# Kernel optimization log

Hardware: AMD Instinct MI355X
Metric: run time of the kernel (lower is better)

The kernel has to match this reference:

```python
import jax, jax.numpy as jnp
import numpy as np

SEQ_LEN = 1
INPUT = 2048
HIDDEN = 2048
CLASSES = 10
K = int(np.floor(np.sqrt(HIDDEN)))            # avgKernelSize = 45
NUM_EH = (HIDDEN - K) // K + 1                # 45 pooled features
LENGTHS = (32, 128, 512)                      # EHlengths (window sizes)
EST_DIM = NUM_EH * len(LENGTHS) * 2           # mean + variance per (feature, window)
B = 8192


def setup_inputs() -> dict:
    key = jax.random.key(0)
    ks = jax.random.split(key, 7)
    s = 1.0 / np.sqrt(HIDDEN)
    u = lambda k, shape: jax.random.uniform(k, shape, jnp.float32, -s, s)
    return {
        "x": jax.random.normal(ks[0], (B, SEQ_LEN, INPUT), jnp.float32),
        "W_ih": u(ks[1], (HIDDEN, INPUT)),
        "W_hh": u(ks[2], (HIDDEN, HIDDEN)),
        "b_ih": u(ks[3], (HIDDEN,)),
        "b_hh": u(ks[4], (HIDDEN,)),
        "W_lin": u(ks[5], (CLASSES, HIDDEN + EST_DIM)),
        "b_lin": u(ks[6], (CLASSES,)),
    }


def _sliding_stats(pooled):
    """Causal sliding-window mean/variance over the batch/stream axis.

    pooled: (B, F). Returns (B, F, J, 2) with [..., 0]=mean, [..., 1]=var.
    This is the exact quantity the VarEH exponential histograms approximate
    (streaming mean/variance over the last L elements added).
    """
    n = pooled.shape[0]
    cs = jnp.cumsum(pooled, axis=0)
    cs2 = jnp.cumsum(pooled * pooled, axis=0)
    idx = jnp.arange(n)
    outs = []
    for L in LENGTHS:  # small fixed set of window lengths
        zpad = jnp.zeros((L,) + pooled.shape[1:], pooled.dtype)
        cs_l = jnp.concatenate([zpad, cs], axis=0)[:n]
        cs2_l = jnp.concatenate([zpad, cs2], axis=0)[:n]
        cnt = jnp.minimum(idx + 1, L).astype(pooled.dtype)[:, None]
        m = (cs - cs_l) / cnt
        v = (cs2 - cs2_l) / cnt - m * m
        outs.append(jnp.stack([m, v], axis=-1))  # (B, F, 2)
    return jnp.stack(outs, axis=2)  # (B, F, J, 2)


def reference(x, W_ih, W_hh, b_ih, b_hh, W_lin, b_lin):
    b = x.shape[0]
    # Elman RNN, batch_first, h0 = 0. Precompute input projection for all steps.
    xw = jnp.einsum("bsi,hi->bsh", x, W_ih) + b_ih + b_hh  # (B, S, H)

    def step(h, xt):
        h = jnp.tanh(xt + h @ W_hh.T)
        return h, h

    h0 = jnp.zeros((b, HIDDEN), x.dtype)
    _, hs = jax.lax.scan(step, h0, jnp.swapaxes(xw, 0, 1))  # (S, B, H)
    rnn_out = hs[-1]  # (B, H); with seq_len=1 this equals squeeze(rnn_out)

    # AvgPool1d(kernel=K, stride=K) over hidden dim -> (B, NUM_EH)
    pooled = rnn_out[:, : NUM_EH * K].reshape(b, NUM_EH, K).mean(axis=-1)

    # Streaming mean/var estimates across the batch stream (VarEH semantics)
    est = _sliding_stats(pooled).reshape(b, EST_DIM)

    lin_in = jnp.concatenate([rnn_out, est], axis=1)  # (B, H + EST_DIM)
    logits = lin_in @ W_lin.T + b_lin
    return jax.nn.softmax(logits, axis=1)
```

## Files before the change

### kernel.cpp

```cpp
#include <hip/hip_runtime.h>
#include <hip/hip_bf16.h>
#include <math.h>

typedef short s16x8 __attribute__((ext_vector_type(8)));
typedef float f32x4 __attribute__((ext_vector_type(4)));

__device__ inline unsigned short f2bf(float x) {
    unsigned int u = __float_as_uint(x);
    unsigned int r = (u + 0x7fffu + ((u >> 16) & 1u)) >> 16;
    return (unsigned short)r;
}
__device__ inline float bf2f(unsigned short u) {
    return __uint_as_float(((unsigned int)u) << 16);
}

__device__ inline float fast_tanh(float x) {
    float e = __expf(2.0f * x);
    return 1.0f - 2.0f * __builtin_amdgcn_rcpf(e + 1.0f);
}

__global__ void cvtprep_kernel(const float* __restrict__ x,
                               const float* __restrict__ W_ih,
                               const float* __restrict__ W_lin,
                               unsigned short* __restrict__ xb,
                               unsigned short* __restrict__ wb,
                               unsigned short* __restrict__ wlb) {
    int blk = blockIdx.x;
    int tid = threadIdx.x;
    if (blk < 16384) {
        int i = blk * 256 + tid;
        float4 v = ((const float4*)x)[i];
        ushort4 o; o.x = f2bf(v.x); o.y = f2bf(v.y); o.z = f2bf(v.z); o.w = f2bf(v.w);
        ((ushort4*)xb)[i] = o;
    } else if (blk < 20480) {
        int i = (blk - 16384) * 256 + tid;
        float4 v = ((const float4*)W_ih)[i];
        ushort4 o; o.x = f2bf(v.x); o.y = f2bf(v.y); o.z = f2bf(v.z); o.w = f2bf(v.w);
        ((ushort4*)wb)[i] = o;
    } else {
        int idx = (blk - 20480) * 256 + tid;
        if (idx < 37376) {
            int c = idx / 2336, k = idx - c * 2336;
            float v = (c < 10 && k < 2318) ? W_lin[c * 2318 + k] : 0.f;
            wlb[idx] = f2bf(v);
        }
    }
}

__global__ __launch_bounds__(256) void gemm_tanh_kernel(
    const unsigned short* __restrict__ A, const unsigned short* __restrict__ Bm,
    const float* __restrict__ b_ih, const float* __restrict__ b_hh,
    unsigned short* __restrict__ Hb)
{
    __shared__ unsigned short As[128 * 32];
    __shared__ unsigned short Bs[128 * 32];

    const int tid  = threadIdx.x;
    const int lane = tid & 63;
    const int wave = tid >> 6;
    const int row0 = blockIdx.x * 128;
    const int col0 = blockIdx.y * 128;
    const int wr = (wave >> 1) * 64;
    const int wc = (wave & 1) * 64;
    const int quad = lane >> 4;
    const int mrow = lane & 15;

    f32x4 acc[4][4];
#pragma unroll
    for (int i = 0; i < 4; ++i)
#pragma unroll
        for (int j = 0; j < 4; ++j)
            acc[i][j] = f32x4{0.f, 0.f, 0.f, 0.f};

    for (int k0 = 0; k0 < 2048; k0 += 32) {
        __syncthreads();
#pragma unroll
        for (int i = 0; i < 2; ++i) {
            int t = i * 256 + tid;
            int r = t >> 2, c = t & 3;
            int cg = c ^ ((r >> 1) & 3);
            const unsigned short* gp = A + (size_t)(row0 + r) * 2048 + k0 + cg * 8;
            __builtin_amdgcn_global_load_lds(
                (const __attribute__((address_space(1))) void*)gp,
                (__attribute__((address_space(3))) void*)(&As[t * 8]), 16, 0, 0);
        }
#pragma unroll
        for (int i = 0; i < 2; ++i) {
            int t = i * 256 + tid;
            int r = t >> 2, c = t & 3;
            int cg = c ^ ((r >> 1) & 3);
            const unsigned short* gp = Bm + (size_t)(col0 + r) * 2048 + k0 + cg * 8;
            __builtin_amdgcn_global_load_lds(
                (const __attribute__((address_space(1))) void*)gp,
                (__attribute__((address_space(3))) void*)(&Bs[t * 8]), 16, 0, 0);
        }
        __syncthreads();

        s16x8 af[4], bfr[4];
#pragma unroll
        for (int i = 0; i < 4; ++i) {
            int R = wr + i * 16 + mrow;
            int slot = quad ^ ((R >> 1) & 3);
            af[i] = *(const s16x8*)(&As[R * 32 + slot * 8]);
        }
#pragma unroll
        for (int j = 0; j < 4; ++j) {
            int R = wc + j * 16 + mrow;
            int slot = quad ^ ((R >> 1) & 3);
            bfr[j] = *(const s16x8*)(&Bs[R * 32 + slot * 8]);
        }
#pragma unroll
        for (int i = 0; i < 4; ++i)
#pragma unroll
            for (int j = 0; j < 4; ++j)
                acc[i][j] = __builtin_amdgcn_mfma_f32_16x16x32_bf16(
                    af[i], bfr[j], acc[i][j], 0, 0, 0);
    }

    float bias[4];
#pragma unroll
    for (int j = 0; j < 4; ++j) {
        int gc = col0 + wc + j * 16 + mrow;
        bias[j] = b_ih[gc] + b_hh[gc];
    }
#pragma unroll
    for (int i = 0; i < 4; ++i) {
#pragma unroll
        for (int r = 0; r < 4; ++r) {
            int grow = row0 + wr + i * 16 + quad * 4 + r;
#pragma unroll
            for (int j = 0; j < 4; ++j) {
                int gc = col0 + wc + j * 16 + mrow;
                float v = acc[i][j][r] + bias[j];
                Hb[(size_t)grow * 2048 + gc] = f2bf(fast_tanh(v));
            }
        }
    }
}

__global__ __launch_bounds__(256) void pool_kernel(
    const unsigned short* __restrict__ Hb, float* __restrict__ pooled_t) {
    __shared__ unsigned short hs[8 * 2048];
    __shared__ float outs[45 * 8];
    int b0 = blockIdx.x * 8;
    int tid = threadIdx.x;
    const ushort4* src = (const ushort4*)(Hb + (size_t)b0 * 2048);
    ushort4* dst = (ushort4*)hs;
    for (int i = tid; i < 4096; i += 256) dst[i] = src[i];
    __syncthreads();
    for (int o = tid; o < 360; o += 256) {
        int f = o % 45, r = o / 45;
        const unsigned short* row = hs + r * 2048 + f * 45;
        float s = 0.f;
#pragma unroll
        for (int k = 0; k < 45; ++k) s += bf2f(row[k]);
        outs[f * 8 + r] = s * (1.0f / 45.0f);
    }
    __syncthreads();
    for (int o = tid; o < 360; o += 256) {
        int f = o >> 3, r = o & 7;
        pooled_t[f * 8192 + b0 + r] = outs[o];
    }
}

__global__ __launch_bounds__(256) void scan_kernel(
    const float* __restrict__ pooled_t,
    float* __restrict__ cs_t, float* __restrict__ cs2_t) {
    __shared__ float t1[256], t2[256];
    int f = blockIdx.x;
    int tid = threadIdx.x;
    const float* p = pooled_t + f * 8192;
    int base = tid * 32;
    float loc[32];
    float s1 = 0.f, s2 = 0.f;
#pragma unroll
    for (int i = 0; i < 32; ++i) {
        float v = p[base + i];
        loc[i] = v; s1 += v; s2 += v * v;
    }
    t1[tid] = s1; t2[tid] = s2;
    __syncthreads();
    for (int d = 1; d < 256; d <<= 1) {
        float a1 = (tid >= d) ? t1[tid - d] : 0.f;
        float a2 = (tid >= d) ? t2[tid - d] : 0.f;
        __syncthreads();
        t1[tid] += a1; t2[tid] += a2;
        __syncthreads();
    }
    float r1 = t1[tid] - s1, r2 = t2[tid] - s2;
    float* c1 = cs_t + f * 8192;
    float* c2 = cs2_t + f * 8192;
#pragma unroll
    for (int i = 0; i < 32; ++i) {
        float v = loc[i];
        r1 += v; r2 += v * v;
        c1[base + i] = r1; c2[base + i] = r2;
    }
}

#define ESTRIDE 290
__global__ __launch_bounds__(256) void final_kernel(
    const unsigned short* __restrict__ Hb,
    const float* __restrict__ cs_t, const float* __restrict__ cs2_t,
    const unsigned short* __restrict__ Wb, const float* __restrict__ b_lin,
    float* __restrict__ out) {
    __shared__ unsigned short Es[32 * ESTRIDE];
    __shared__ float comb[2 * 16 * 17];
    int tid = threadIdx.x;
    int lane = tid & 63;
    int wave = tid >> 6;
    int b0 = blockIdx.x * 32;

    for (int i = tid; i < 135 * 32; i += 256) {
        int fj = i >> 5, r = i & 31;
        int f = fj / 3, j = fj - 3 * f;
        int b = b0 + r;
        int L = (j == 0) ? 32 : (j == 1) ? 128 : 512;
        const float* c1 = cs_t + f * 8192;
        const float* c2 = cs2_t + f * 8192;
        float a1 = c1[b], a2 = c2[b];
        float p1 = 0.f, p2 = 0.f;
        if (b >= L) { p1 = c1[b - L]; p2 = c2[b - L]; }
        float cnt = (float)((b + 1 < L) ? (b + 1) : L);
        float m = (a1 - p1) / cnt;
        float v = (a2 - p2) / cnt - m * m;
        int d0 = f * 6 + j * 2;
        Es[r * ESTRIDE + d0]     = f2bf(m);
        Es[r * ESTRIDE + d0 + 1] = f2bf(v);
    }
    for (int i = tid; i < 32 * 18; i += 256) {
        int r = i / 18, d = 270 + i % 18;
        Es[r * ESTRIDE + d] = 0;
    }
    __syncthreads();

    const int t = wave >> 1;
    const int kh = wave & 1;
    const int quad = lane >> 4;
    const int mrow = lane & 15;
    const int rowt = b0 + t * 16;

    f32x4 acc = f32x4{0.f, 0.f, 0.f, 0.f};
    const unsigned short* arow = Hb + (size_t)(rowt + mrow) * 2048 + kh * 1024 + quad * 8;
    const unsigned short* brow = Wb + (size_t)mrow * 2336 + kh * 1024 + quad * 8;
#pragma unroll 4
    for (int k = 0; k < 1024; k += 32) {
        s16x8 a = *(const s16x8*)(arow + k);
        s16x8 b = *(const s16x8*)(brow + k);
        acc = __builtin_amdgcn_mfma_f32_16x16x32_bf16(a, b, acc, 0, 0, 0);
    }
    if (kh) {
        const unsigned short* erow = Es + (t * 16 + mrow) * ESTRIDE + quad * 8;
        const unsigned short* wrow = Wb + (size_t)mrow * 2336 + 2048 + quad * 8;
#pragma unroll
        for (int k = 0; k < 288; k += 32) {
            s16x8 a = *(const s16x8*)(erow + k);
            s16x8 b = *(const s16x8*)(wrow + k);
            acc = __builtin_amdgcn_mfma_f32_16x16x32_bf16(a, b, acc, 0, 0, 0);
        }
    }

    float* cb = comb + t * 272;
    if (kh == 0) {
#pragma unroll
        for (int r = 0; r < 4; ++r) cb[(quad * 4 + r) * 17 + mrow] = acc[r];
    }
    __syncthreads();
    if (kh == 1) {
#pragma unroll
        for (int r = 0; r < 4; ++r) cb[(quad * 4 + r) * 17 + mrow] += acc[r];
    }
    __syncthreads();

    if (tid < 32) {
        const float* base = comb + (tid >> 4) * 272 + (tid & 15) * 17;
        float lg[10];
        float mx = -1e30f;
#pragma unroll
        for (int c = 0; c < 10; ++c) {
            lg[c] = base[c] + b_lin[c];
            mx = fmaxf(mx, lg[c]);
        }
        float s = 0.f;
#pragma unroll
        for (int c = 0; c < 10; ++c) { lg[c] = expf(lg[c] - mx); s += lg[c]; }
        float inv = 1.0f / s;
#pragma unroll
        for (int c = 0; c < 10; ++c) out[(size_t)(b0 + tid) * 10 + c] = lg[c] * inv;
    }
}

extern "C" void kernel_launch(void* const* d_in, const int* in_sizes, int n_in,
                              void* d_out, int out_size, void* d_ws, size_t ws_size,
                              hipStream_t stream) {
    const float* x     = (const float*)d_in[0];
    const float* W_ih  = (const float*)d_in[1];
    const float* b_ih  = (const float*)d_in[3];
    const float* b_hh  = (const float*)d_in[4];
    const float* W_lin = (const float*)d_in[5];
    const float* b_lin = (const float*)d_in[6];
    float* out = (float*)d_out;

    char* ws = (char*)d_ws;
    unsigned short* xb  = (unsigned short*)(ws);
    unsigned short* wb  = (unsigned short*)(ws + 33554432);
    unsigned short* Hb  = (unsigned short*)(ws + 41943040);
    float* pooled_t     = (float*)(ws + 75497472);
    float* cs_t         = (float*)(ws + 76972032);
    float* cs2_t        = (float*)(ws + 78446592);
    unsigned short* wlb = (unsigned short*)(ws + 79921152);

    cvtprep_kernel<<<20626, 256, 0, stream>>>(x, W_ih, W_lin, xb, wb, wlb);
    dim3 ggrid(64, 16);
    gemm_tanh_kernel<<<ggrid, 256, 0, stream>>>(xb, wb, b_ih, b_hh, Hb);
    pool_kernel<<<1024, 256, 0, stream>>>(Hb, pooled_t);
    scan_kernel<<<45, 256, 0, stream>>>(pooled_t, cs_t, cs2_t);
    final_kernel<<<256, 256, 0, stream>>>(Hb, cs_t, cs2_t, wlb, b_lin, out);
}
```

Before: 253.2 us.

## Rewrite RNN input GEMM as 256x256 double-buffered pipelined MFMA kernel

```diff
diff --git a/kernel.cpp b/kernel.cpp
--- a/kernel.cpp
+++ b/kernel.cpp
@@ -47,91 +47,171 @@
     }
 }
 
-__global__ __launch_bounds__(256) void gemm_tanh_kernel(
+
+#define MFMA_(a, b, c) __builtin_amdgcn_mfma_f32_16x16x32_bf16(a, b, c, 0, 0, 0)
+
+__device__ inline s16x8 frag_ld(const unsigned short* hbase, int row, int ksub, int quad) {
+    int slot = (ksub * 4 + quad) ^ (row & 7);
+    return *(const s16x8*)(hbase + row * 64 + slot * 8);
+}
+
+__device__ inline void stage_u(const unsigned short* __restrict__ gmat, int half,
+                               int rowoff, int kt, unsigned short* lmat, int tid) {
+    int r = tid >> 3, s = tid & 7;
+    int lr = rowoff + r;
+    int ks = (s ^ (lr & 7)) << 3;
+    const unsigned short* gp = gmat + (size_t)(half * 128 + lr) * 2048 + kt * 64 + ks;
+    __builtin_amdgcn_global_load_lds(
+        (const __attribute__((address_space(1))) void*)gp,
+        (__attribute__((address_space(3))) void*)(lmat + half * 8192 + lr * 64 + s * 8),
+        16, 0, 0);
+}
+
+#define LOAD_AQ(q)                                                       \
+    af0 = frag_ld(Ah, (q) * 32 +      mrow, 0, quad);                    \
+    af1 = frag_ld(Ah, (q) * 32 + 16 + mrow, 0, quad);                    \
+    af2 = frag_ld(Ah, (q) * 32 +      mrow, 1, quad);                    \
+    af3 = frag_ld(Ah, (q) * 32 + 16 + mrow, 1, quad);
+
+#define MFMA_Q(q)                                                        \
+    acc[(q)*2 + 0][0] = MFMA_(af0, bf00, acc[(q)*2 + 0][0]);             \
+    acc[(q)*2 + 0][1] = MFMA_(af0, bf01, acc[(q)*2 + 0][1]);             \
+    acc[(q)*2 + 0][2] = MFMA_(af0, bf02, acc[(q)*2 + 0][2]);             \
+    acc[(q)*2 + 0][3] = MFMA_(af0, bf03, acc[(q)*2 + 0][3]);             \
+    acc[(q)*2 + 1][0] = MFMA_(af1, bf00, acc[(q)*2 + 1][0]);             \
+    acc[(q)*2 + 1][1] = MFMA_(af1, bf01, acc[(q)*2 + 1][1]);             \
+    acc[(q)*2 + 1][2] = MFMA_(af1, bf02, acc[(q)*2 + 1][2]);             \
+    acc[(q)*2 + 1][3] = MFMA_(af1, bf03, acc[(q)*2 + 1][3]);             \
+    acc[(q)*2 + 0][0] = MFMA_(af2, bf10, acc[(q)*2 + 0][0]);             \
+    acc[(q)*2 + 0][1] = MFMA_(af2, bf11, acc[(q)*2 + 0][1]);             \
+    acc[(q)*2 + 0][2] = MFMA_(af2, bf12, acc[(q)*2 + 0][2]);             \
+    acc[(q)*2 + 0][3] = MFMA_(af2, bf13, acc[(q)*2 + 0][3]);             \
+    acc[(q)*2 + 1][0] = MFMA_(af3, bf10, acc[(q)*2 + 1][0]);             \
+    acc[(q)*2 + 1][1] = MFMA_(af3, bf11, acc[(q)*2 + 1][1]);             \
+    acc[(q)*2 + 1][2] = MFMA_(af3, bf12, acc[(q)*2 + 1][2]);             \
+    acc[(q)*2 + 1][3] = MFMA_(af3, bf13, acc[(q)*2 + 1][3]);
+
+#define PHASE_CORE(q)                                                    \
+    __builtin_amdgcn_s_barrier();                                        \
+    asm volatile("s_waitcnt lgkmcnt(0)" ::: "memory");                   \
+    __builtin_amdgcn_s_setprio(1);                                       \
+    MFMA_Q(q);                                                           \
+    __builtin_amdgcn_s_setprio(0);
+
+__global__ __launch_bounds__(512) void gemm_tanh_kernel(
     const unsigned short* __restrict__ A, const unsigned short* __restrict__ Bm,
     const float* __restrict__ b_ih, const float* __restrict__ b_hh,
     unsigned short* __restrict__ Hb)
 {
-    __shared__ unsigned short As[128 * 32];
-    __shared__ unsigned short Bs[128 * 32];
+    __shared__ __align__(16) unsigned short lds[2][2][16384];
 
     const int tid  = threadIdx.x;
     const int lane = tid & 63;
     const int wave = tid >> 6;
-    const int row0 = blockIdx.x * 128;
-    const int col0 = blockIdx.y * 128;
-    const int wr = (wave >> 1) * 64;
-    const int wc = (wave & 1) * 64;
+    const int wgid = blockIdx.x;
+    const int cblk = wgid & 7;
+    const int rblk = wgid >> 3;
+    const int row0 = rblk * 256;
+    const int col0 = cblk * 256;
+    const int wm   = wave >> 2;
+    const int wn   = wave & 3;
     const int quad = lane >> 4;
     const int mrow = lane & 15;
-
-    f32x4 acc[4][4];
-#pragma unroll
-    for (int i = 0; i < 4; ++i)
-#pragma unroll
-        for (int j = 0; j < 4; ++j)
-            acc[i][j] = f32x4{0.f, 0.f, 0.f, 0.f};
-
-    for (int k0 = 0; k0 < 2048; k0 += 32) {
-        __syncthreads();
-#pragma unroll
-        for (int i = 0; i < 2; ++i) {
-            int t = i * 256 + tid;
-            int r = t >> 2, c = t & 3;
-            int cg = c ^ ((r >> 1) & 3);
-            const unsigned short* gp = A + (size_t)(row0 + r) * 2048 + k0 + cg * 8;
-            __builtin_amdgcn_global_load_lds(
-                (const __attribute__((address_space(1))) void*)gp,
-                (__attribute__((address_space(3))) void*)(&As[t * 8]), 16, 0, 0);
-        }
-#pragma unroll
-        for (int i = 0; i < 2; ++i) {
-            int t = i * 256 + tid;
-            int r = t >> 2, c = t & 3;
-            int cg = c ^ ((r >> 1) & 3);
-            const unsigned short* gp = Bm + (size_t)(col0 + r) * 2048 + k0 + cg * 8;
-            __builtin_amdgcn_global_load_lds(
-                (const __attribute__((address_space(1))) void*)gp,
-                (__attribute__((address_space(3))) void*)(&Bs[t * 8]), 16, 0, 0);
-        }
-        __syncthreads();
-
-        s16x8 af[4], bfr[4];
-#pragma unroll
-        for (int i = 0; i < 4; ++i) {
-            int R = wr + i * 16 + mrow;
-            int slot = quad ^ ((R >> 1) & 3);
-            af[i] = *(const s16x8*)(&As[R * 32 + slot * 8]);
-        }
-#pragma unroll
-        for (int j = 0; j < 4; ++j) {
-            int R = wc + j * 16 + mrow;
-            int slot = quad ^ ((R >> 1) & 3);
-            bfr[j] = *(const s16x8*)(&Bs[R * 32 + slot * 8]);
-        }
-#pragma unroll
-        for (int i = 0; i < 4; ++i)
-#pragma unroll
-            for (int j = 0; j < 4; ++j)
-                acc[i][j] = __builtin_amdgcn_mfma_f32_16x16x32_bf16(
-                    af[i], bfr[j], acc[i][j], 0, 0, 0);
+    const int NT   = 32;
+
+    const unsigned short* Ag = A  + (size_t)row0 * 2048;
+    const unsigned short* Bg = Bm + (size_t)col0 * 2048;
+
+    f32x4 acc[8][4];
+#pragma unroll
+    for (int i = 0; i < 8; ++i)
+#pragma unroll
+        for (int j = 0; j < 4; ++j) acc[i][j] = f32x4{0.f, 0.f, 0.f, 0.f};
+
+    stage_u(Ag, 0, 0,  0, lds[0][0], tid);  stage_u(Ag, 0, 64, 0, lds[0][0], tid);
+    stage_u(Ag, 1, 0,  0, lds[0][0], tid);  stage_u(Ag, 1, 64, 0, lds[0][0], tid);
+    stage_u(Bg, 0, 0,  0, lds[0][1], tid);  stage_u(Bg, 0, 64, 0, lds[0][1], tid);
+    stage_u(Bg, 1, 0,  0, lds[0][1], tid);  stage_u(Bg, 1, 64, 0, lds[0][1], tid);
+    stage_u(Bg, 0, 0,  1, lds[1][1], tid);  stage_u(Bg, 0, 64, 1, lds[1][1], tid);
+    stage_u(Bg, 1, 0,  1, lds[1][1], tid);  stage_u(Bg, 1, 64, 1, lds[1][1], tid);
+    stage_u(Ag, 0, 0,  1, lds[1][0], tid);  stage_u(Ag, 1, 0,  1, lds[1][0], tid);
+    asm volatile("s_waitcnt vmcnt(6)" ::: "memory");
+    __builtin_amdgcn_s_barrier();
+
+    for (int t = 0; t < NT; ++t) {
+        const int buf = t & 1;
+        unsigned short* LA  = lds[buf][0];
+        unsigned short* LB  = lds[buf][1];
+        unsigned short* NLA = lds[buf ^ 1][0];
+        const unsigned short* Ah = LA + wm * 8192;
+        const unsigned short* Bh = LB + (wn >> 1) * 8192;
+        const int bco = (wn & 1) * 64;
+
+        s16x8 bf00, bf01, bf02, bf03, bf10, bf11, bf12, bf13;
+        s16x8 af0, af1, af2, af3;
+
+        bf00 = frag_ld(Bh, bco +  0 + mrow, 0, quad);
+        bf01 = frag_ld(Bh, bco + 16 + mrow, 0, quad);
+        bf02 = frag_ld(Bh, bco + 32 + mrow, 0, quad);
+        bf03 = frag_ld(Bh, bco + 48 + mrow, 0, quad);
+        bf10 = frag_ld(Bh, bco +  0 + mrow, 1, quad);
+        bf11 = frag_ld(Bh, bco + 16 + mrow, 1, quad);
+        bf12 = frag_ld(Bh, bco + 32 + mrow, 1, quad);
+        bf13 = frag_ld(Bh, bco + 48 + mrow, 1, quad);
+        LOAD_AQ(0);
+        if (t + 1 < NT) {
+            stage_u(Ag, 0, 64, t + 1, NLA, tid);
+            stage_u(Ag, 1, 64, t + 1, NLA, tid);
+        }
+        asm volatile("s_waitcnt lgkmcnt(8)" ::: "memory");
+        PHASE_CORE(0);
+        __builtin_amdgcn_s_barrier();
+
+        LOAD_AQ(1);
+        if (t + 2 < NT) {
+            stage_u(Bg, 0, 0,  t + 2, LB, tid);
+            stage_u(Bg, 0, 64, t + 2, LB, tid);
+        }
+        PHASE_CORE(1);
+        __builtin_amdgcn_s_barrier();
+
+        LOAD_AQ(2);
+        if (t + 2 < NT) {
+            stage_u(Bg, 1, 0,  t + 2, LB, tid);
+            stage_u(Bg, 1, 64, t + 2, LB, tid);
+        }
+        PHASE_CORE(2);
+        __builtin_amdgcn_s_barrier();
+
+        LOAD_AQ(3);
+        if (t + 2 < NT) {
+            stage_u(Ag, 0, 0, t + 2, LA, tid);
+            stage_u(Ag, 1, 0, t + 2, LA, tid);
+        }
+        PHASE_CORE(3);
+        if (t + 2 < NT) {
+            asm volatile("s_waitcnt vmcnt(6)" ::: "memory");
+        } else if (t + 1 < NT) {
+            asm volatile("s_waitcnt vmcnt(0)" ::: "memory");
+        }
+        __builtin_amdgcn_s_barrier();
     }
 
     float bias[4];
 #pragma unroll
     for (int j = 0; j < 4; ++j) {
-        int gc = col0 + wc + j * 16 + mrow;
+        int gc = col0 + wn * 64 + j * 16 + mrow;
         bias[j] = b_ih[gc] + b_hh[gc];
     }
 #pragma unroll
-    for (int i = 0; i < 4; ++i) {
-#pragma unroll
-        for (int r = 0; r < 4; ++r) {
-            int grow = row0 + wr + i * 16 + quad * 4 + r;
+    for (int i = 0; i < 8; ++i) {
+#pragma unroll
+        for (int rr = 0; rr < 4; ++rr) {
+            int grow = row0 + wm * 128 + i * 16 + quad * 4 + rr;
 #pragma unroll
             for (int j = 0; j < 4; ++j) {
-                int gc = col0 + wc + j * 16 + mrow;
-                float v = acc[i][j][r] + bias[j];
+                int gc = col0 + wn * 64 + j * 16 + mrow;
+                float v = acc[i][j][rr] + bias[j];
                 Hb[(size_t)grow * 2048 + gc] = f2bf(fast_tanh(v));
             }
         }
@@ -311,8 +391,7 @@
     unsigned short* wlb = (unsigned short*)(ws + 79921152);
 
     cvtprep_kernel<<<20626, 256, 0, stream>>>(x, W_ih, W_lin, xb, wb, wlb);
-    dim3 ggrid(64, 16);
-    gemm_tanh_kernel<<<ggrid, 256, 0, stream>>>(xb, wb, b_ih, b_hh, Hb);
+    gemm_tanh_kernel<<<256, 512, 0, stream>>>(xb, wb, b_ih, b_hh, Hb);
     pool_kernel<<<1024, 256, 0, stream>>>(Hb, pooled_t);
     scan_kernel<<<45, 256, 0, stream>>>(pooled_t, cs_t, cs2_t);
     final_kernel<<<256, 256, 0, stream>>>(Hb, cs_t, cs2_t, wlb, b_lin, out);
```

Measured after the change: 224.3 us. 1.13x faster.
